# Kernel tuning notes

Hardware: AMD Instinct MI355X
Metric: run time of the kernel (lower is better)

## Reference

```python
import jax, jax.numpy as jnp
import numpy as np

HDR_H, HDR_W = 16, 32  # HDR_map_shape[:2]


def _light_dirs_and_coeff():
    # Matl: unit direction per HDR texel, matching the torch double loop.
    phi = (jnp.arange(HDR_H, dtype=jnp.float32) / HDR_H) * jnp.pi          # (16,)
    theta = (jnp.arange(HDR_W, dtype=jnp.float32) / HDR_W) * (2 * jnp.pi)  # (32,)
    sp, cp = jnp.sin(phi)[:, None], jnp.cos(phi)[:, None]                  # (16,1)
    st, ct = jnp.sin(theta)[None, :], jnp.cos(theta)[None, :]              # (1,32)
    dirs = jnp.stack([st * sp, jnp.broadcast_to(cp, (HDR_H, HDR_W)), -ct * sp], axis=-1)  # (16,32,3)
    dirs = dirs / jnp.linalg.norm(dirs, axis=-1, keepdims=True)
    Matl = dirs.reshape(-1, 3).T                                            # (3, M=512)
    coeff = jnp.broadcast_to(sp[:, :, None], (HDR_H, 1, 3))                 # (16,1,3), sin(phi) per row
    return Matl, coeff


def setup_inputs() -> dict:
    key = jax.random.key(0)
    k1, k2, k3 = jax.random.split(key, 3)
    B, H, W = 2, 512, 512
    env = jax.random.uniform(k1, (B, HDR_H, HDR_W, 3), dtype=jnp.float32)
    normal = jax.random.uniform(k2, (B, H, W, 3), dtype=jnp.float32)
    albedo = jax.random.uniform(k3, (B, 3, H, W), dtype=jnp.float32)
    return {"env": env, "normal": normal, "albedo": albedo}


def reference(env, normal, albedo):
    B, H, W, _ = normal.shape
    Matl, coeff = _light_dirs_and_coeff()
    # HDR weighting: env * sin(phi) row coefficient -> (B, M, 3)
    hdr = (env * coeff[None]).reshape(B, HDR_H * HDR_W, 3)
    # Normal map: flip channel order (::-1) then decode to [-1,1]
    n = (normal[..., ::-1] - 0.5) * 2.0
    Matn = n.reshape(B, H * W, 3)                                           # (B, N, 3)
    # relu-clamped dot products against all light directions: (B, N, M)
    Matd = jax.nn.relu(jnp.einsum('bnk,km->bnm', Matn, Matl))
    # weight by HDR and reduce over light directions (same math as the per-channel torch loop)
    light = jnp.einsum('bnm,bmc->bnc', Matd, hdr)                           # (B, N, 3)
    lightmap = light.reshape(B, H, W, 3).transpose(0, 3, 1, 2)              # (B, 3, H, W)
    diffuse = (lightmap / 50.0) * albedo
    return diffuse
```

## Files before the change

kernel.cpp:

```cpp
#include <hip/hip_runtime.h>


constexpr int HW     = 512 * 512;
constexpr int WAVES  = 4;
constexpr int GROUPS = 8;

typedef _Float16 half2v __attribute__((ext_vector_type(2)));
typedef _Float16 half8  __attribute__((ext_vector_type(8)));
typedef float    f32x4  __attribute__((ext_vector_type(4)));

__device__ constexpr float SPc[8] = {
    0.195090322f, 0.382683432f, 0.555570233f, 0.707106781f,
    0.831469612f, 0.923879533f, 0.980785280f, 1.0f };
__device__ constexpr float CPc[8] = {
    0.980785280f, 0.923879533f, 0.831469612f, 0.707106781f,
    0.555570233f, 0.382683432f, 0.195090322f, 0.0f };
__device__ constexpr float STc[32] = {
    0.0f,          0.195090322f,  0.382683432f,  0.555570233f,
    0.707106781f,  0.831469612f,  0.923879533f,  0.980785280f,
    1.0f,          0.980785280f,  0.923879533f,  0.831469612f,
    0.707106781f,  0.555570233f,  0.382683432f,  0.195090322f,
    0.0f,         -0.195090322f, -0.382683432f, -0.555570233f,
   -0.707106781f, -0.831469612f, -0.923879533f, -0.980785280f,
   -1.0f,         -0.980785280f, -0.923879533f, -0.831469612f,
   -0.707106781f, -0.555570233f, -0.382683432f, -0.195090322f };

union h8u { unsigned u[4]; half8 v; half2v h2[4]; };

__global__ __launch_bounds__(256, 4)
void env_render_fused(const float* __restrict__ env,
                      const float* __restrict__ normal,
                      const float* __restrict__ albedo,
                      float* __restrict__ out)
{
    __shared__ float lds_env[16 * 32 * 3];
    __shared__ half8 lds_hf[512];
    __shared__ float lds_nrm[WAVES][GROUPS * 48];
    __shared__ float lds_light[WAVES][GROUPS * 48];
    __shared__ float Wred[WAVES][9];

    const int b    = blockIdx.y;
    const int t    = threadIdx.x;
    const int lane = t & 63, wave = t >> 6;
    const int ch   = lane & 15, cg = lane >> 4;

    const int wavepx0 = (blockIdx.x * WAVES + wave) * (GROUPS * 16);

    #pragma unroll
    for (int q = 0; q < 6; ++q)
        lds_env[t + q * 256] = env[(size_t)b * 1536 + t + q * 256];

    {
        const float* nsrc = normal + ((size_t)b * HW + wavepx0) * 3;
        const f32x4 v = *(const f32x4*)(nsrc + lane * 4);
        *(f32x4*)&lds_nrm[wave][lane * 4] = v;
        const float2 w = *(const float2*)(nsrc + 256 + lane * 2);
        *(float2*)&lds_nrm[wave][256 + lane * 2] = w;
    }
    __syncthreads();

    #pragma unroll
    for (int ss = 0; ss < 2; ++ss) {
        const int s = t + ss * 256;
        const int tile = s >> 6, ln = s & 63;
        const int kc = ln >> 4, chh = ln & 15;
        const int j  = tile * 4 + kc;
        half8 f;
        #pragma unroll
        for (int e = 0; e < 8; ++e) {
            const int i = e + 1;
            float v = 0.f;
            if (chh < 3 && !(i == 8 && j >= 16)) {
                const int i2 = 16 - i, j2 = (j + 16) & 31;
                v = (lds_env[(i * 32 + j) * 3 + chh] +
                     lds_env[(i2 * 32 + j2) * 3 + chh]) * (SPc[e] * 0.01f);
            }
            f[e] = (_Float16)v;
        }
        lds_hf[s] = f;
    }

    float W[9];
    #pragma unroll
    for (int q = 0; q < 9; ++q) W[q] = 0.0f;
    if (t < 240) {
        int i, j;
        if (t < 224) { i = 1 + (t >> 5); j = t & 31; }
        else         { i = 8;            j = t - 224; }
        const int i2 = 16 - i, j2 = (j + 16) & 31;
        const float sp = SPc[i - 1], cp = CPc[i - 1];
        const float st = STc[j], ct = STc[(j + 8) & 31];
        const float dx = st * sp, dy = cp, dz = -ct * sp;
        const float scale = sp * 0.01f;
        const float* ea = lds_env + (i * 32 + j) * 3;
        const float* eb = lds_env + (i2 * 32 + j2) * 3;
        const float hd0 = (ea[0] - eb[0]) * scale;
        const float hd1 = (ea[1] - eb[1]) * scale;
        const float hd2 = (ea[2] - eb[2]) * scale;
        W[0] = dx * hd0; W[1] = dx * hd1; W[2] = dx * hd2;
        W[3] = dy * hd0; W[4] = dy * hd1; W[5] = dy * hd2;
        W[6] = dz * hd0; W[7] = dz * hd1; W[8] = dz * hd2;
    }
    #pragma unroll
    for (int q = 0; q < 9; ++q) {
        float v = W[q];
        #pragma unroll
        for (int off = 32; off > 0; off >>= 1) v += __shfl_down(v, off);
        if (lane == 0) Wred[wave][q] = v;
    }
    __syncthreads();

    float Wl[9];
    #pragma unroll
    for (int q = 0; q < 9; ++q)
        Wl[q] = Wred[0][q] + Wred[1][q] + Wred[2][q] + Wred[3][q];

    half8 Hf[8];
    #pragma unroll
    for (int tl = 0; tl < 8; ++tl) Hf[tl] = lds_hf[tl * 64 + lane];

    half2v st2[4], ct2[4], sp2[4], cp2[4];
    #pragma unroll
    for (int p = 0; p < 4; ++p) {
        const int ja = (2 * p) * 4 + cg, jb = (2 * p + 1) * 4 + cg;
        st2[p] = half2v{(_Float16)STc[ja], (_Float16)STc[jb]};
        ct2[p] = half2v{(_Float16)STc[(ja + 8) & 31], (_Float16)STc[(jb + 8) & 31]};
        sp2[p] = half2v{(_Float16)SPc[2 * p], (_Float16)SPc[2 * p + 1]};
        cp2[p] = half2v{(_Float16)CPc[2 * p], (_Float16)CPc[2 * p + 1]};
    }

    #pragma unroll
    for (int g = 0; g < GROUPS; ++g) {
        const int pxl = g * 16 + ch;
        const float n0 = lds_nrm[wave][pxl * 3 + 0];
        const float n1 = lds_nrm[wave][pxl * 3 + 1];
        const float n2 = lds_nrm[wave][pxl * 3 + 2];
        const float nx = fmaf(n2, 2.0f, -1.0f);
        const float ny = fmaf(n1, 2.0f, -1.0f);
        const float nz = fmaf(n0, 2.0f, -1.0f);

        const _Float16 nxh = (_Float16)nx, nyh = (_Float16)ny, nzh = (_Float16)nz;
        const half2v nx2 = {nxh, nxh}, ny2 = {nyh, nyh}, nz2 = {nzh, nzh};

        half2v u2[4], nyc2[4];
        #pragma unroll
        for (int p = 0; p < 4; ++p) {
            u2[p]   = nx2 * st2[p] - nz2 * ct2[p];
            nyc2[p] = ny2 * cp2[p];
        }

        f32x4 acc = {0.f, 0.f, 0.f, 0.f};
        #pragma unroll
        for (int tl = 0; tl < 8; ++tl) {
            const _Float16 uh = (tl & 1) ? u2[tl >> 1].y : u2[tl >> 1].x;
            const half2v ub = {uh, uh};
            h8u pk;
            #pragma unroll
            for (int p = 0; p < 4; ++p) {
                const half2v d2 = sp2[p] * ub + nyc2[p];
                pk.h2[p] = d2;
                pk.u[p] &= 0x7FFF7FFFu;
            }
            acc = __builtin_amdgcn_mfma_f32_16x16x32_f16(Hf[tl], pk.v, acc, 0, 0, 0);
        }

        if (cg == 0) {
            lds_light[wave][pxl]                   = acc[0] + fmaf(nx, Wl[0], fmaf(ny, Wl[3], nz * Wl[6]));
            lds_light[wave][GROUPS * 16 + pxl]     = acc[1] + fmaf(nx, Wl[1], fmaf(ny, Wl[4], nz * Wl[7]));
            lds_light[wave][GROUPS * 32 + pxl]     = acc[2] + fmaf(nx, Wl[2], fmaf(ny, Wl[5], nz * Wl[8]));
        }
    }
    __syncthreads();

    const size_t bbase = (size_t)b * 3 * HW + wavepx0;
    #pragma unroll
    for (int c = 0; c < 3; ++c) {
        const f32x4 av = *(const f32x4*)(albedo + bbase + (size_t)c * HW + lane * 2
                                         - (lane & 1) * 2);
        (void)av;
        break;
    }
    #pragma unroll
    for (int c = 0; c < 3; ++c) {
        const size_t o = bbase + (size_t)c * HW + lane * 2;
        const float2 av = *(const float2*)(albedo + o);
        const float2 lv = *(const float2*)&lds_light[wave][c * GROUPS * 16 + lane * 2];
        float2 ov; ov.x = av.x * lv.x; ov.y = av.y * lv.y;
        *(float2*)(out + o) = ov;
    }
}

extern "C" void kernel_launch(void* const* d_in, const int* in_sizes, int n_in,
                              void* d_out, int out_size, void* d_ws, size_t ws_size,
                              hipStream_t stream)
{
    const float* env    = (const float*)d_in[0];
    const float* normal = (const float*)d_in[1];
    const float* albedo = (const float*)d_in[2];
    float* out          = (float*)d_out;

    const int B = in_sizes[0] / (16 * 32 * 3);

    dim3 grid(HW / (WAVES * GROUPS * 16), B);
    env_render_fused<<<grid, 256, 0, stream>>>(env, normal, albedo, out);
}
```

Baseline: 17.89 us.

## Prefetch albedo into LDS asynchronously and split MFMA accumulator chains

The albedo tile for each block is now issued as direct global-to-LDS loads before the MFMA loop, so its memory latency can overlap the lighting computation instead of being paid at the epilogue. The epilogue reads albedo from LDS. The single MFMA accumulator is also split into two independent chains to cut back-to-back dependency stalls. The cost is 6 KB more LDS per block, which may lower occupancy, and it relies on the barrier before the epilogue to cover completion of the async loads.

```diff
diff --git a/kernel.cpp b/kernel.cpp
--- a/kernel.cpp
+++ b/kernel.cpp
@@ -37,6 +37,7 @@
     __shared__ half8 lds_hf[512];
     __shared__ float lds_nrm[WAVES][GROUPS * 48];
     __shared__ float lds_light[WAVES][GROUPS * 48];
+    __shared__ float lds_alb[3 * 512];
     __shared__ float Wred[WAVES][9];
 
     const int b    = blockIdx.y;
@@ -44,7 +45,8 @@
     const int lane = t & 63, wave = t >> 6;
     const int ch   = lane & 15, cg = lane >> 4;
 
-    const int wavepx0 = (blockIdx.x * WAVES + wave) * (GROUPS * 16);
+    const int blockpx0 = blockIdx.x * (WAVES * GROUPS * 16);
+    const int wavepx0  = blockpx0 + wave * (GROUPS * 16);
 
     #pragma unroll
     for (int q = 0; q < 6; ++q)
@@ -110,6 +112,25 @@
     }
     __syncthreads();
 
+    {
+        const int s0 = wave;
+        const float* g0 = albedo + ((size_t)b * 3 + (s0 >> 1)) * HW
+                          + blockpx0 + (s0 & 1) * 256 + lane * 4;
+        __builtin_amdgcn_global_load_lds(
+            (const __attribute__((address_space(1))) unsigned*)g0,
+            (__attribute__((address_space(3))) unsigned*)&lds_alb[s0 * 256 + lane * 4],
+            16, 0, 0);
+        if (wave < 2) {
+            const int s1 = wave + 4;
+            const float* g1 = albedo + ((size_t)b * 3 + (s1 >> 1)) * HW
+                              + blockpx0 + (s1 & 1) * 256 + lane * 4;
+            __builtin_amdgcn_global_load_lds(
+                (const __attribute__((address_space(1))) unsigned*)g1,
+                (__attribute__((address_space(3))) unsigned*)&lds_alb[s1 * 256 + lane * 4],
+                16, 0, 0);
+        }
+    }
+
     float Wl[9];
     #pragma unroll
     for (int q = 0; q < 9; ++q)
@@ -149,7 +170,8 @@
             nyc2[p] = ny2 * cp2[p];
         }
 
-        f32x4 acc = {0.f, 0.f, 0.f, 0.f};
+        f32x4 acc0 = {0.f, 0.f, 0.f, 0.f};
+        f32x4 acc1 = {0.f, 0.f, 0.f, 0.f};
         #pragma unroll
         for (int tl = 0; tl < 8; ++tl) {
             const _Float16 uh = (tl & 1) ? u2[tl >> 1].y : u2[tl >> 1].x;
@@ -161,29 +183,24 @@
                 pk.h2[p] = d2;
                 pk.u[p] &= 0x7FFF7FFFu;
             }
-            acc = __builtin_amdgcn_mfma_f32_16x16x32_f16(Hf[tl], pk.v, acc, 0, 0, 0);
+            if (tl < 4) acc0 = __builtin_amdgcn_mfma_f32_16x16x32_f16(Hf[tl], pk.v, acc0, 0, 0, 0);
+            else        acc1 = __builtin_amdgcn_mfma_f32_16x16x32_f16(Hf[tl], pk.v, acc1, 0, 0, 0);
         }
 
         if (cg == 0) {
-            lds_light[wave][pxl]                   = acc[0] + fmaf(nx, Wl[0], fmaf(ny, Wl[3], nz * Wl[6]));
-            lds_light[wave][GROUPS * 16 + pxl]     = acc[1] + fmaf(nx, Wl[1], fmaf(ny, Wl[4], nz * Wl[7]));
-            lds_light[wave][GROUPS * 32 + pxl]     = acc[2] + fmaf(nx, Wl[2], fmaf(ny, Wl[5], nz * Wl[8]));
+            lds_light[wave][pxl]               = acc0[0] + acc1[0] + fmaf(nx, Wl[0], fmaf(ny, Wl[3], nz * Wl[6]));
+            lds_light[wave][GROUPS * 16 + pxl] = acc0[1] + acc1[1] + fmaf(nx, Wl[1], fmaf(ny, Wl[4], nz * Wl[7]));
+            lds_light[wave][GROUPS * 32 + pxl] = acc0[2] + acc1[2] + fmaf(nx, Wl[2], fmaf(ny, Wl[5], nz * Wl[8]));
         }
     }
     __syncthreads();
 
     const size_t bbase = (size_t)b * 3 * HW + wavepx0;
-    #pragma unroll
-    for (int c = 0; c < 3; ++c) {
-        const f32x4 av = *(const f32x4*)(albedo + bbase + (size_t)c * HW + lane * 2
-                                         - (lane & 1) * 2);
-        (void)av;
-        break;
-    }
+    const int wloc = wave * (GROUPS * 16);
     #pragma unroll
     for (int c = 0; c < 3; ++c) {
         const size_t o = bbase + (size_t)c * HW + lane * 2;
-        const float2 av = *(const float2*)(albedo + o);
+        const float2 av = *(const float2*)&lds_alb[c * 512 + wloc + lane * 2];
         const float2 lv = *(const float2*)&lds_light[wave][c * GROUPS * 16 + lane * 2];
         float2 ov; ov.x = av.x * lv.x; ov.y = av.y * lv.y;
         *(float2*)(out + o) = ov;
```

Result: slower. 18.44 us (+3.1%).
